# Performance work log

Measured on AMD Instinct MI355X. Metric: run time of the kernel, lower is better.

## Reference

```python
import jax, jax.numpy as jnp
import numpy as np

B, C, H, W = 16, 256, 56, 56
PH, PW = 7, 7            # partition (window) size
HEADS, DH = 8, 32        # n_heads = C // head_dim
P = PH * PW              # tokens per window = 49
GH, GW = H // PH, W // PW
G = GH * GW              # number of windows = 64
MLP = 4                  # mlp_ratio
EPS = 1e-5
SCALE = C ** (-0.5)      # note: torch code scales by feat_dim, not head_dim


def _rel_index(h, w):
    coords = np.stack(np.meshgrid(np.arange(h), np.arange(w), indexing='ij'))  # [2,h,w]
    cf = coords.reshape(2, -1)
    rel = cf[:, :, None] - cf[:, None, :]              # [2,P,P]
    rel = rel.transpose(1, 2, 0)
    rel[:, :, 0] += h - 1
    rel[:, :, 1] += w - 1
    rel[:, :, 0] *= 2 * w - 1
    return rel.sum(-1).astype(np.int32)                # [P,P]


def setup_inputs() -> dict:
    key = jax.random.key(0)
    ks = jax.random.split(key, 8)
    std = 0.02
    return {
        'x': jax.random.normal(ks[0], (B, C, H, W), jnp.float32),
        'ln1_g': jnp.ones((C,), jnp.float32),
        'ln1_b': jnp.zeros((C,), jnp.float32),
        'wqkv': jax.random.normal(ks[1], (C, 3 * C), jnp.float32) * std,
        'bqkv': jnp.zeros((3 * C,), jnp.float32),
        'wmerge': jax.random.normal(ks[2], (C, C), jnp.float32) * std,
        'bmerge': jnp.zeros((C,), jnp.float32),
        'bias_table': jax.random.normal(ks[3], ((2 * PH - 1) * (2 * PW - 1), HEADS), jnp.float32) * std,
        'ln2_g': jnp.ones((C,), jnp.float32),
        'ln2_b': jnp.zeros((C,), jnp.float32),
        'w1': jax.random.normal(ks[4], (C, MLP * C), jnp.float32) * std,
        'b1': jnp.zeros((MLP * C,), jnp.float32),
        'w2': jax.random.normal(ks[5], (MLP * C, C), jnp.float32) * std,
        'b2': jnp.zeros((C,), jnp.float32),
        'rel_idx': jnp.asarray(_rel_index(PH, PW)),
    }


def _layernorm(x, g, b):
    mu = jnp.mean(x, axis=-1, keepdims=True)
    var = jnp.var(x, axis=-1, keepdims=True)
    return (x - mu) * jax.lax.rsqrt(var + EPS) * g + b


def reference(x, ln1_g, ln1_b, wqkv, bqkv, wmerge, bmerge, bias_table,
              ln2_g, ln2_b, w1, b1, w2, b2, rel_idx):
    # --- window partition: [B,C,H,W] -> [B,G,P,C]
    xw = x.reshape(B, C, GH, PH, GW, PW).transpose(0, 2, 4, 3, 5, 1).reshape(B, G, P, C)

    # --- relative-position attention block
    y = _layernorm(xw, ln1_g, ln1_b)
    qkv = y @ wqkv + bqkv                               # [B,G,P,3C]
    q, k, v = jnp.split(qkv, 3, axis=-1)
    q = q.reshape(B, G, P, HEADS, DH)
    k = k.reshape(B, G, P, HEADS, DH) * SCALE
    v = v.reshape(B, G, P, HEADS, DH)
    scores = jnp.einsum('bgihd,bgjhd->bghij', q, k)     # [B,G,H,P,P]
    bias = bias_table[rel_idx].transpose(2, 0, 1)       # [H,P,P]
    attn = jax.nn.softmax(scores + bias[None, None], axis=-1)
    out = jnp.einsum('bghij,bgjhd->bgihd', attn, v).reshape(B, G, P, C)
    out = out @ wmerge + bmerge
    xw = xw + out

    # --- MLP block
    z = _layernorm(xw, ln2_g, ln2_b)
    z = jax.nn.gelu(z @ w1 + b1, approximate=False) @ w2 + b2
    xw = xw + z

    # --- window departition: [B,G,P,C] -> [B,C,H,W]
    xo = xw.reshape(B, GH, GW, PH, PW, C).transpose(0, 5, 1, 3, 2, 4).reshape(B, C, H, W)
    return xo
```

## Files before the change

kernel.cpp:

```cpp
#include <hip/hip_runtime.h>
#include <hip/hip_bf16.h>

#define B_      16
#define C_      256
#define H_      56
#define W_      56
#define HW_     3136
#define G_      64
#define P_      49
#define NTOK    50176
#define HEADS_  8
#define DH_     32
#define SCALE_  0.0625f
#define EPS_    1e-5f

typedef short bf16x8 __attribute__((ext_vector_type(8)));
typedef short bf16x4_t __attribute__((ext_vector_type(4)));
typedef float f32x4  __attribute__((ext_vector_type(4)));
using bf16 = __hip_bfloat16;

__device__ __forceinline__ void gload16(const void* g, void* l) {
  __builtin_amdgcn_global_load_lds((const __attribute__((address_space(1))) void*)g,
                                   (__attribute__((address_space(3))) void*)l, 16, 0, 0);
}
__device__ __forceinline__ float b2f(short s) {
  union { float f; unsigned u; } v; v.u = ((unsigned)(unsigned short)s) << 16; return v.f;
}
__device__ __forceinline__ short f2b(float f) {
  union { float f; unsigned u; } v; v.f = f;
  unsigned r = (v.u + 0x7FFFu + ((v.u >> 16) & 1u)) >> 16;
  return (short)r;
}

__global__ __launch_bounds__(256)
void prep_kernel(const float* __restrict__ wqkv, const float* __restrict__ wmerge,
                 const float* __restrict__ w1, const float* __restrict__ w2,
                 const float* __restrict__ btab, const int* __restrict__ relidx,
                 bf16* __restrict__ wqkvT, bf16* __restrict__ wmergeT,
                 bf16* __restrict__ w1T, bf16* __restrict__ w2T,
                 short* __restrict__ bt)
{
  int idx = blockIdx.x * 256 + threadIdx.x;
  if (idx < 196608) { int n = idx >> 8, k = idx & 255;
    wqkvT[idx] = __float2bfloat16(wqkv[k * 768 + n]); return; }
  idx -= 196608;
  if (idx < 65536) { int n = idx >> 8, k = idx & 255;
    wmergeT[idx] = __float2bfloat16(wmerge[k * 256 + n]); return; }
  idx -= 65536;
  if (idx < 262144) { int n = idx >> 8, k = idx & 255;
    w1T[idx] = __float2bfloat16(w1[k * 1024 + n]); return; }
  idx -= 262144;
  if (idx < 262144) { int n = idx >> 10, k = idx & 1023;
    w2T[idx] = __float2bfloat16(w2[k * 256 + n]); return; }
  idx -= 262144;
  if (idx < 32768) {
    int h = idx >> 12, rest = idx & 4095;
    int key = rest >> 6, col = rest & 63;
    int q = col >> 2, qni = col & 3;
    int query = qni * 16 + q;
    float v = 0.f;
    if (key < P_ && query < P_) v = btab[relidx[query * P_ + key] * HEADS_ + h];
    bt[idx] = f2b(v);
  }
}

__global__ __launch_bounds__(256)
void ingest_kernel(const float* __restrict__ x, const float* __restrict__ gam,
                   const float* __restrict__ bet, short* __restrict__ xtok,
                   short* __restrict__ y)
{
  __shared__ short Lt[56 * 260];
  const int h = blockIdx.x % 56, b = blockIdx.x / 56;
  const int tid = threadIdx.x;

  const float* xb = x + (size_t)b * 256 * HW_ + h * 56;
#pragma unroll
  for (int i = 0; i < 14; i++) {
    int idx = i * 256 + tid;
    int c = idx / 14, w4 = idx - c * 14;
    float4 v = *(const float4*)(xb + (size_t)c * HW_ + w4 * 4);
    Lt[(w4 * 4 + 0) * 260 + c] = f2b(v.x);
    Lt[(w4 * 4 + 1) * 260 + c] = f2b(v.y);
    Lt[(w4 * 4 + 2) * 260 + c] = f2b(v.z);
    Lt[(w4 * 4 + 3) * 260 + c] = f2b(v.w);
  }
  __syncthreads();

  const int lane = tid & 63, wv = tid >> 6;
  float4 gv = *(const float4*)(gam + lane * 4);
  float4 bv = *(const float4*)(bet + lane * 4);
  const int hdiv = h / 7, hmod = h - hdiv * 7;

  for (int t = 0; t < 14; t++) {
    int w = wv * 14 + t;
    bf16x4_t raw = *(const bf16x4_t*)&Lt[w * 260 + lane * 4];
    float f0 = b2f(raw[0]), f1 = b2f(raw[1]), f2 = b2f(raw[2]), f3 = b2f(raw[3]);
    float sum = f0 + f1 + f2 + f3;
    float sq  = f0*f0 + f1*f1 + f2*f2 + f3*f3;
#pragma unroll
    for (int off = 32; off > 0; off >>= 1) {
      sum += __shfl_xor(sum, off, 64);
      sq  += __shfl_xor(sq,  off, 64);
    }
    float mu = sum * (1.0f / 256.0f);
    float var = sq * (1.0f / 256.0f) - mu * mu;
    float rs = rsqrtf(var + EPS_);
    int wdiv = w / 7, wmod = w - wdiv * 7;
    int tok = b * HW_ + (hdiv * 8 + wdiv) * P_ + hmod * 7 + wmod;
    *(bf16x4_t*)(xtok + (size_t)tok * 256 + lane * 4) = raw;
    bf16x4_t o;
    o[0] = f2b((f0 - mu) * rs * gv.x + bv.x);
    o[1] = f2b((f1 - mu) * rs * gv.y + bv.y);
    o[2] = f2b((f2 - mu) * rs * gv.z + bv.z);
    o[3] = f2b((f3 - mu) * rs * gv.w + bv.w);
    *(bf16x4_t*)(y + (size_t)tok * 256 + lane * 4) = o;
  }
}

__global__ __launch_bounds__(256)
void egress_kernel(const short* __restrict__ outtok, float* __restrict__ out)
{
  const int h = blockIdx.x % 56, b = blockIdx.x / 56;
  const int w = threadIdx.x & 63, cblk = threadIdx.x >> 6;
  const bool act = w < 56;
  const int wcl = act ? w : 55;
  const int tok = b * HW_ + ((h / 7) * 8 + wcl / 7) * P_ + (h % 7) * 7 + (wcl % 7);
  const short* src = outtok + (size_t)tok * 256 + cblk * 64;
  float* dst = out + ((size_t)b * 256 + cblk * 64) * HW_ + h * 56 + w;
#pragma unroll
  for (int j0 = 0; j0 < 64; j0 += 8) {
    bf16x8 r = *(const bf16x8*)(src + j0);
#pragma unroll
    for (int jj = 0; jj < 8; jj++)
      if (act) dst[(size_t)(j0 + jj) * HW_] = b2f(r[jj]);
  }
}

__global__ __launch_bounds__(64)
void attn_kernel(const short* __restrict__ qkv, const short* __restrict__ bt,
                 short* __restrict__ out)
{
  __shared__ short Pbuf[64 * 72];
  const int bid = blockIdx.x;
  const int h = bid & 7;
  const int t0 = (bid >> 3) * P_;
  const int lane = threadIdx.x;
  const int g = lane >> 4, q = lane & 15;

  const short* qb = qkv + (size_t)t0 * 768 + h * 32;

  bf16x8 vf[2][2];
#pragma unroll
  for (int kkt = 0; kkt < 2; kkt++)
#pragma unroll
    for (int n2 = 0; n2 < 2; n2++)
#pragma unroll
      for (int jj = 0; jj < 8; jj++) {
        int key = kkt * 32 + 8 * g + jj; key = key > 48 ? 48 : key;
        vf[kkt][n2][jj] = qb[(size_t)key * 768 + 512 + n2 * 16 + q];
      }

  bf16x8 kf[4], qf[4];
#pragma unroll
  for (int mi = 0; mi < 4; mi++) {
    int r_ = mi * 16 + q; r_ = r_ > 48 ? 48 : r_;
    kf[mi] = *(const bf16x8*)(qb + (size_t)r_ * 768 + 256 + 8 * g);
  }
#pragma unroll
  for (int ni = 0; ni < 4; ni++) {
    int r_ = ni * 16 + q; r_ = r_ > 48 ? 48 : r_;
    qf[ni] = *(const bf16x8*)(qb + (size_t)r_ * 768 + 8 * g);
  }

  f32x4 sacc[4][4] = {};
#pragma unroll
  for (int mi = 0; mi < 4; mi++)
#pragma unroll
    for (int ni = 0; ni < 4; ni++)
      sacc[mi][ni] = __builtin_amdgcn_mfma_f32_16x16x32_bf16(kf[mi], qf[ni], sacc[mi][ni], 0, 0, 0);

  float mx[4] = {-1e30f, -1e30f, -1e30f, -1e30f};
  const short* btb = bt + (size_t)(h * 64) * 64 + q * 4;
#pragma unroll
  for (int mi = 0; mi < 4; mi++)
#pragma unroll
    for (int r = 0; r < 4; r++) {
      int key = mi * 16 + 4 * g + r;
      bf16x4_t bv = *(const bf16x4_t*)(btb + key * 64);
      bool valid = key < P_;
#pragma unroll
      for (int ni = 0; ni < 4; ni++) {
        float s = valid ? fmaf(sacc[mi][ni][r], SCALE_, b2f(bv[ni])) : -1e30f;
        sacc[mi][ni][r] = s;
        mx[ni] = fmaxf(mx[ni], s);
      }
    }
#pragma unroll
  for (int ni = 0; ni < 4; ni++) {
    mx[ni] = fmaxf(mx[ni], __shfl_xor(mx[ni], 16, 64));
    mx[ni] = fmaxf(mx[ni], __shfl_xor(mx[ni], 32, 64));
  }
  float sm[4] = {0.f, 0.f, 0.f, 0.f};
#pragma unroll
  for (int mi = 0; mi < 4; mi++)
#pragma unroll
    for (int ni = 0; ni < 4; ni++)
#pragma unroll
      for (int r = 0; r < 4; r++) {
        float p = __expf(sacc[mi][ni][r] - mx[ni]);
        sacc[mi][ni][r] = p;
        sm[ni] += p;
      }
#pragma unroll
  for (int ni = 0; ni < 4; ni++) {
    sm[ni] += __shfl_xor(sm[ni], 16, 64);
    sm[ni] += __shfl_xor(sm[ni], 32, 64);
    sm[ni] = 1.0f / sm[ni];
  }
#pragma unroll
  for (int ni = 0; ni < 4; ni++)
#pragma unroll
    for (int mi = 0; mi < 4; mi++) {
      bf16x4_t pv;
#pragma unroll
      for (int r = 0; r < 4; r++) pv[r] = f2b(sacc[mi][ni][r] * sm[ni]);
      *(bf16x4_t*)&Pbuf[(ni * 16 + q) * 72 + mi * 16 + 4 * g] = pv;
    }
  __syncthreads();

  f32x4 oacc[4][2] = {};
#pragma unroll
  for (int kkt = 0; kkt < 2; kkt++) {
    bf16x8 paf[4];
#pragma unroll
    for (int qi = 0; qi < 4; qi++)
      paf[qi] = *(const bf16x8*)&Pbuf[(qi * 16 + q) * 72 + kkt * 32 + 8 * g];
#pragma unroll
    for (int qi = 0; qi < 4; qi++)
#pragma unroll
      for (int n2 = 0; n2 < 2; n2++)
        oacc[qi][n2] = __builtin_amdgcn_mfma_f32_16x16x32_bf16(paf[qi], vf[kkt][n2], oacc[qi][n2], 0, 0, 0);
  }

  short* ob = out + (size_t)t0 * 256 + h * 32;
#pragma unroll
  for (int qi = 0; qi < 4; qi++)
#pragma unroll
    for (int r = 0; r < 4; r++) {
      int query = qi * 16 + 4 * g + r;
      if (query < P_) {
#pragma unroll
        for (int n2 = 0; n2 < 2; n2++)
          ob[(size_t)query * 256 + n2 * 16 + q] = f2b(oacc[qi][n2][r]);
      }
    }
}

template<int EPI, int WR, int WN>
__global__ __launch_bounds__(WR * WN * 64)
void gemm_kernel(const bf16* __restrict__ A, const bf16* __restrict__ Wt,
                 const float* __restrict__ bias, int N, int K,
                 bf16* __restrict__ outb, short* __restrict__ res_io,
                 short* __restrict__ z_out,
                 const float* __restrict__ gam, const float* __restrict__ bet)
{
  constexpr int THREADS = WR * WN * 64;
  constexpr int BM = WR * 64, BN = WN * 64;
  constexpr int RPP = THREADS / 4;
  constexpr int APASS = BM / RPP > 0 ? BM / RPP : 1;
  constexpr int BPASS = BN / RPP > 0 ? BN / RPP : 1;
  __shared__ __align__(16) bf16 As[2][BM * 32];
  __shared__ __align__(16) bf16 Bs[2][BN * 32];
  __shared__ float red1[(EPI == 3) ? 64 : 1][(EPI == 3) ? WN : 1];
  __shared__ float red2[(EPI == 3) ? 64 : 1][(EPI == 3) ? WN : 1];

  const int tid = threadIdx.x;
  const int lane = tid & 63;
  const int wave = tid >> 6;
  const int wr = wave / WN, wc = wave % WN;

  int bx = blockIdx.x, by = blockIdx.y;
  {
    const int gx = gridDim.x, gy = gridDim.y;
    if (gx > 1) {
      int hwid = blockIdx.x + gx * blockIdx.y;
      int band = gx * 8;
      int fullb = gy >> 3;
      int full = fullb * band;
      if (hwid < full) {
        int g8 = hwid / band, w = hwid % band;
        by = g8 * 8 + (w & 7); bx = w >> 3;
      } else {
        int rem = gy & 7;
        int w = hwid - full;
        by = fullb * 8 + w % rem; bx = w / rem;
      }
    }
  }
  const int bm = by * BM, bn = bx * BN;

  f32x4 acc[4][4] = {};

  const int trow = tid >> 2;
  const int tcol = ((tid & 3) ^ ((tid >> 3) & 3)) * 8;
  const bf16* aA[APASS];
  const bf16* aB[BPASS];
#pragma unroll
  for (int p = 0; p < APASS; p++)
    aA[p] = A + (size_t)(bm + p * RPP + trow) * K + tcol;
#pragma unroll
  for (int p = 0; p < BPASS; p++)
    aB[p] = Wt + (size_t)(bn + p * RPP + trow) * K + tcol;
  const int dOff = tid * 8;

  const int kc_sw = ((lane >> 4) ^ ((lane >> 1) & 3)) * 8;
  const int l15 = lane & 15, g = lane >> 4;
  const int rA = wr * 64 + l15;
  const int rB = wc * 64 + l15;

  const int nt = K >> 5;

#pragma unroll
  for (int p = 0; p < APASS; p++) gload16(aA[p], &As[0][p * RPP * 32 + dOff]);
#pragma unroll
  for (int p = 0; p < BPASS; p++) gload16(aB[p], &Bs[0][p * RPP * 32 + dOff]);
  __syncthreads();

  for (int t = 0; t < nt; ++t) {
    const int cur = t & 1;
    if (t + 1 < nt) {
      const int k1 = (t + 1) << 5;
      const int nxt = cur ^ 1;
#pragma unroll
      for (int p = 0; p < APASS; p++) gload16(aA[p] + k1, &As[nxt][p * RPP * 32 + dOff]);
#pragma unroll
      for (int p = 0; p < BPASS; p++) gload16(aB[p] + k1, &Bs[nxt][p * RPP * 32 + dOff]);
    }
    bf16x8 af[4], bfr[4];
#pragma unroll
    for (int i = 0; i < 4; i++) {
      af[i]  = *(const bf16x8*)(&As[cur][(rA + i * 16) * 32 + kc_sw]);
      bfr[i] = *(const bf16x8*)(&Bs[cur][(rB + i * 16) * 32 + kc_sw]);
    }
#pragma unroll
    for (int mi = 0; mi < 4; mi++)
#pragma unroll
      for (int ni = 0; ni < 4; ni++)
        acc[mi][ni] = __builtin_amdgcn_mfma_f32_16x16x32_bf16(af[mi], bfr[ni], acc[mi][ni], 0, 0, 0);
    __syncthreads();
  }

  if constexpr (EPI == 3) {
    const int ocol0 = wc * 64;
    float bv[4], gv[4], btv[4];
#pragma unroll
    for (int ni = 0; ni < 4; ni++) {
      bv[ni]  = bias[ocol0 + ni * 16 + l15];
      gv[ni]  = gam[ocol0 + ni * 16 + l15];
      btv[ni] = bet[ocol0 + ni * 16 + l15];
    }
#pragma unroll
    for (int mi = 0; mi < 4; mi++)
#pragma unroll
      for (int r = 0; r < 4; r++) {
        const int rowl = mi * 16 + g * 4 + r;
        float s1 = 0.f, s2 = 0.f;
#pragma unroll
        for (int ni = 0; ni < 4; ni++) {
          const int col = ocol0 + ni * 16 + l15;
          float v = acc[mi][ni][r] + bv[ni]
                  + b2f(res_io[(size_t)(bm + rowl) * 256 + col]);
          acc[mi][ni][r] = v;
          s1 += v; s2 += v * v;
        }
#pragma unroll
        for (int off = 1; off < 16; off <<= 1) {
          s1 += __shfl_xor(s1, off, 64);
          s2 += __shfl_xor(s2, off, 64);
        }
        if (l15 == 0) { red1[rowl][wc] = s1; red2[rowl][wc] = s2; }
      }
    __syncthreads();
#pragma unroll
    for (int mi = 0; mi < 4; mi++)
#pragma unroll
      for (int r = 0; r < 4; r++) {
        const int rowl = mi * 16 + g * 4 + r;
        float m1 = 0.f, m2 = 0.f;
#pragma unroll
        for (int j = 0; j < WN; j++) { m1 += red1[rowl][j]; m2 += red2[rowl][j]; }
        float mu = m1 * (1.0f / 256.0f);
        float var = m2 * (1.0f / 256.0f) - mu * mu;
        float rs = rsqrtf(var + EPS_);
#pragma unroll
        for (int ni = 0; ni < 4; ni++) {
          const int col = ocol0 + ni * 16 + l15;
          float v = acc[mi][ni][r];
          res_io[(size_t)(bm + rowl) * 256 + col] = f2b(v);
          z_out [(size_t)(bm + rowl) * 256 + col] = f2b((v - mu) * rs * gv[ni] + btv[ni]);
        }
      }
    return;
  }

#pragma unroll
  for (int mi = 0; mi < 4; mi++) {
#pragma unroll
    for (int ni = 0; ni < 4; ni++) {
#pragma unroll
      for (int r = 0; r < 4; r++) {
        const int row = bm + wr * 64 + mi * 16 + g * 4 + r;
        const int col = bn + wc * 64 + ni * 16 + l15;
        float v = acc[mi][ni][r] + bias[col];
        if (EPI == 0) {
          outb[(size_t)row * N + col] = __float2bfloat16(v);
        } else if (EPI == 1) {
          float u = 0.7978845608f * v * (1.0f + 0.044715f * v * v);
          float e = __expf(2.0f * u);
          float th = 1.0f - 2.0f / (e + 1.0f);
          outb[(size_t)row * N + col] = __float2bfloat16(0.5f * v * (1.0f + th));
        } else {
          size_t o = (size_t)row * 256 + col;
          res_io[o] = f2b(v + b2f(res_io[o]));
        }
      }
    }
  }
}

extern "C" void kernel_launch(void* const* d_in, const int* in_sizes, int n_in,
                              void* d_out, int out_size, void* d_ws, size_t ws_size,
                              hipStream_t stream)
{
  const float* x      = (const float*)d_in[0];
  const float* ln1_g  = (const float*)d_in[1];
  const float* ln1_b  = (const float*)d_in[2];
  const float* wqkv   = (const float*)d_in[3];
  const float* bqkv   = (const float*)d_in[4];
  const float* wmerge = (const float*)d_in[5];
  const float* bmerge = (const float*)d_in[6];
  const float* btab   = (const float*)d_in[7];
  const float* ln2_g  = (const float*)d_in[8];
  const float* ln2_b  = (const float*)d_in[9];
  const float* w1     = (const float*)d_in[10];
  const float* b1     = (const float*)d_in[11];
  const float* w2     = (const float*)d_in[12];
  const float* b2     = (const float*)d_in[13];
  const int*   relidx = (const int*)d_in[14];
  float* out = (float*)d_out;

  char* ws = (char*)d_ws;
  bf16*  wqkvT   = (bf16*)(ws);
  bf16*  wmergeT = (bf16*)(ws + 393216);
  bf16*  w1T     = (bf16*)(ws + 524288);
  bf16*  w2T     = (bf16*)(ws + 1048576);
  short* battn   = (short*)(ws + 1572864);
  short* R1      = (short*)(ws + 1638400);
  short* R2      = (short*)(ws + 27328512);
  short* qkvc    = (short*)(ws + 53018624);
  short* attnc   = (short*)(ws + 91553792);
  short* hbuf    = (short*)(ws + 53018624);

  prep_kernel<<<3200, 256, 0, stream>>>(wqkv, wmerge, w1, w2, btab, relidx,
                                        wqkvT, wmergeT, w1T, w2T, battn);

  ingest_kernel<<<896, 256, 0, stream>>>(x, ln1_g, ln1_b, R1, R2);

  for (int c = 0; c < 2; ++c) {
    size_t r0 = (size_t)c * 25088;
    gemm_kernel<0, 2, 4><<<dim3(3, 196), 512, 0, stream>>>(
        (const bf16*)(R2 + r0 * 256), wqkvT, bqkv, 768, 256, (bf16*)qkvc,
        nullptr, nullptr, nullptr, nullptr);
    attn_kernel<<<4096, 64, 0, stream>>>(qkvc, battn, attnc);
    gemm_kernel<3, 1, 4><<<dim3(1, 392), 256, 0, stream>>>(
        (const bf16*)attnc, wmergeT, bmerge, 256, 256, nullptr,
        R1 + r0 * 256, R2 + r0 * 256, ln2_g, ln2_b);
  }

  for (int c = 0; c < 2; ++c) {
    size_t r0 = (size_t)c * 25088;
    gemm_kernel<1, 2, 4><<<dim3(4, 196), 512, 0, stream>>>(
        (const bf16*)(R2 + r0 * 256), w1T, b1, 1024, 256, (bf16*)hbuf,
        nullptr, nullptr, nullptr, nullptr);
    gemm_kernel<2, 2, 2><<<dim3(2, 196), 256, 0, stream>>>(
        (const bf16*)hbuf, w2T, b2, 256, 1024, nullptr,
        R1 + r0 * 256, nullptr, nullptr, nullptr);
  }

  egress_kernel<<<896, 256, 0, stream>>>(R1, out);
}
```

Measured before the change: 322.9 us.

## Load GEMM MFMA fragments directly from global memory instead of LDS staging

Result: slower. 481.7 us (+49.2%).

```diff
diff --git a/kernel.cpp b/kernel.cpp
--- a/kernel.cpp
+++ b/kernel.cpp
@@ -19,17 +19,12 @@
 typedef float f32x4  __attribute__((ext_vector_type(4)));
 using bf16 = __hip_bfloat16;
 
-__device__ __forceinline__ void gload16(const void* g, void* l) {
-  __builtin_amdgcn_global_load_lds((const __attribute__((address_space(1))) void*)g,
-                                   (__attribute__((address_space(3))) void*)l, 16, 0, 0);
-}
 __device__ __forceinline__ float b2f(short s) {
   union { float f; unsigned u; } v; v.u = ((unsigned)(unsigned short)s) << 16; return v.f;
 }
 __device__ __forceinline__ short f2b(float f) {
-  union { float f; unsigned u; } v; v.f = f;
-  unsigned r = (v.u + 0x7FFFu + ((v.u >> 16) & 1u)) >> 16;
-  return (short)r;
+  __hip_bfloat16 h = __float2bfloat16(f);
+  return *reinterpret_cast<short*>(&h);
 }
 
 __global__ __launch_bounds__(256)
@@ -256,21 +251,15 @@
     }
 }
 
-template<int EPI, int WR, int WN>
+template<int EPI, int WR, int WN, int K>
 __global__ __launch_bounds__(WR * WN * 64)
 void gemm_kernel(const bf16* __restrict__ A, const bf16* __restrict__ Wt,
-                 const float* __restrict__ bias, int N, int K,
-                 bf16* __restrict__ outb, short* __restrict__ res_io,
-                 short* __restrict__ z_out,
+                 const float* __restrict__ bias, int N,
+                 bf16* __restrict__ outb, bf16* __restrict__ res_io,
+                 bf16* __restrict__ z_out,
                  const float* __restrict__ gam, const float* __restrict__ bet)
 {
-  constexpr int THREADS = WR * WN * 64;
   constexpr int BM = WR * 64, BN = WN * 64;
-  constexpr int RPP = THREADS / 4;
-  constexpr int APASS = BM / RPP > 0 ? BM / RPP : 1;
-  constexpr int BPASS = BN / RPP > 0 ? BN / RPP : 1;
-  __shared__ __align__(16) bf16 As[2][BM * 32];
-  __shared__ __align__(16) bf16 Bs[2][BN * 32];
   __shared__ float red1[(EPI == 3) ? 64 : 1][(EPI == 3) ? WN : 1];
   __shared__ float red2[(EPI == 3) ? 64 : 1][(EPI == 3) ? WN : 1];
 
@@ -278,6 +267,7 @@
   const int lane = tid & 63;
   const int wave = tid >> 6;
   const int wr = wave / WN, wc = wave % WN;
+  const int l15 = lane & 15, g = lane >> 4;
 
   int bx = blockIdx.x, by = blockIdx.y;
   {
@@ -299,55 +289,32 @@
   }
   const int bm = by * BM, bn = bx * BN;
 
+  const bf16* Ap[4];
+  const bf16* Bp[4];
+#pragma unroll
+  for (int mi = 0; mi < 4; mi++)
+    Ap[mi] = A + (size_t)(bm + wr * 64 + mi * 16 + l15) * K + g * 8;
+#pragma unroll
+  for (int ni = 0; ni < 4; ni++)
+    Bp[ni] = Wt + (size_t)(bn + wc * 64 + ni * 16 + l15) * K + g * 8;
+
   f32x4 acc[4][4] = {};
 
-  const int trow = tid >> 2;
-  const int tcol = ((tid & 3) ^ ((tid >> 3) & 3)) * 8;
-  const bf16* aA[APASS];
-  const bf16* aB[BPASS];
-#pragma unroll
-  for (int p = 0; p < APASS; p++)
-    aA[p] = A + (size_t)(bm + p * RPP + trow) * K + tcol;
-#pragma unroll
-  for (int p = 0; p < BPASS; p++)
-    aB[p] = Wt + (size_t)(bn + p * RPP + trow) * K + tcol;
-  const int dOff = tid * 8;
-
-  const int kc_sw = ((lane >> 4) ^ ((lane >> 1) & 3)) * 8;
-  const int l15 = lane & 15, g = lane >> 4;
-  const int rA = wr * 64 + l15;
-  const int rB = wc * 64 + l15;
-
-  const int nt = K >> 5;
-
-#pragma unroll
-  for (int p = 0; p < APASS; p++) gload16(aA[p], &As[0][p * RPP * 32 + dOff]);
-#pragma unroll
-  for (int p = 0; p < BPASS; p++) gload16(aB[p], &Bs[0][p * RPP * 32 + dOff]);
-  __syncthreads();
-
-  for (int t = 0; t < nt; ++t) {
-    const int cur = t & 1;
-    if (t + 1 < nt) {
-      const int k1 = (t + 1) << 5;
-      const int nxt = cur ^ 1;
-#pragma unroll
-      for (int p = 0; p < APASS; p++) gload16(aA[p] + k1, &As[nxt][p * RPP * 32 + dOff]);
-#pragma unroll
-      for (int p = 0; p < BPASS; p++) gload16(aB[p] + k1, &Bs[nxt][p * RPP * 32 + dOff]);
-    }
-    bf16x8 af[4], bfr[4];
-#pragma unroll
-    for (int i = 0; i < 4; i++) {
-      af[i]  = *(const bf16x8*)(&As[cur][(rA + i * 16) * 32 + kc_sw]);
-      bfr[i] = *(const bf16x8*)(&Bs[cur][(rB + i * 16) * 32 + kc_sw]);
-    }
-#pragma unroll
-    for (int mi = 0; mi < 4; mi++)
-#pragma unroll
-      for (int ni = 0; ni < 4; ni++)
-        acc[mi][ni] = __builtin_amdgcn_mfma_f32_16x16x32_bf16(af[mi], bfr[ni], acc[mi][ni], 0, 0, 0);
-    __syncthreads();
+  for (int k0 = 0; k0 < K; k0 += 256) {
+#pragma unroll
+    for (int t = 0; t < 8; ++t) {
+      const int k = k0 + t * 32;
+      bf16x8 af[4], bfr[4];
+#pragma unroll
+      for (int mi = 0; mi < 4; mi++) af[mi] = *(const bf16x8*)(Ap[mi] + k);
+#pragma unroll
+      for (int ni = 0; ni < 4; ni++) bfr[ni] = *(const bf16x8*)(Bp[ni] + k);
+#pragma unroll
+      for (int mi = 0; mi < 4; mi++)
+#pragma unroll
+        for (int ni = 0; ni < 4; ni++)
+          acc[mi][ni] = __builtin_amdgcn_mfma_f32_16x16x32_bf16(af[mi], bfr[ni], acc[mi][ni], 0, 0, 0);
+    }
   }
 
   if constexpr (EPI == 3) {
@@ -369,7 +336,7 @@
         for (int ni = 0; ni < 4; ni++) {
           const int col = ocol0 + ni * 16 + l15;
           float v = acc[mi][ni][r] + bv[ni]
-                  + b2f(res_io[(size_t)(bm + rowl) * 256 + col]);
+                  + __bfloat162float(res_io[(size_t)(bm + rowl) * 256 + col]);
           acc[mi][ni][r] = v;
           s1 += v; s2 += v * v;
         }
@@ -396,8 +363,9 @@
         for (int ni = 0; ni < 4; ni++) {
           const int col = ocol0 + ni * 16 + l15;
           float v = acc[mi][ni][r];
-          res_io[(size_t)(bm + rowl) * 256 + col] = f2b(v);
-          z_out [(size_t)(bm + rowl) * 256 + col] = f2b((v - mu) * rs * gv[ni] + btv[ni]);
+          res_io[(size_t)(bm + rowl) * 256 + col] = __float2bfloat16(v);
+          z_out [(size_t)(bm + rowl) * 256 + col] =
+              __float2bfloat16((v - mu) * rs * gv[ni] + btv[ni]);
         }
       }
     return;
@@ -407,11 +375,12 @@
   for (int mi = 0; mi < 4; mi++) {
 #pragma unroll
     for (int ni = 0; ni < 4; ni++) {
+      const int col = bn + wc * 64 + ni * 16 + l15;
+      const float bv = bias[col];
 #pragma unroll
       for (int r = 0; r < 4; r++) {
         const int row = bm + wr * 64 + mi * 16 + g * 4 + r;
-        const int col = bn + wc * 64 + ni * 16 + l15;
-        float v = acc[mi][ni][r] + bias[col];
+        float v = acc[mi][ni][r] + bv;
         if (EPI == 0) {
           outb[(size_t)row * N + col] = __float2bfloat16(v);
         } else if (EPI == 1) {
@@ -421,7 +390,7 @@
           outb[(size_t)row * N + col] = __float2bfloat16(0.5f * v * (1.0f + th));
         } else {
           size_t o = (size_t)row * 256 + col;
-          res_io[o] = f2b(v + b2f(res_io[o]));
+          res_io[o] = __float2bfloat16(v + __bfloat162float(res_io[o]));
         }
       }
     }
@@ -468,23 +437,23 @@
 
   for (int c = 0; c < 2; ++c) {
     size_t r0 = (size_t)c * 25088;
-    gemm_kernel<0, 2, 4><<<dim3(3, 196), 512, 0, stream>>>(
-        (const bf16*)(R2 + r0 * 256), wqkvT, bqkv, 768, 256, (bf16*)qkvc,
+    gemm_kernel<0, 2, 2, 256><<<dim3(6, 196), 256, 0, stream>>>(
+        (const bf16*)(R2 + r0 * 256), wqkvT, bqkv, 768, (bf16*)qkvc,
         nullptr, nullptr, nullptr, nullptr);
     attn_kernel<<<4096, 64, 0, stream>>>(qkvc, battn, attnc);
-    gemm_kernel<3, 1, 4><<<dim3(1, 392), 256, 0, stream>>>(
-        (const bf16*)attnc, wmergeT, bmerge, 256, 256, nullptr,
-        R1 + r0 * 256, R2 + r0 * 256, ln2_g, ln2_b);
+    gemm_kernel<3, 1, 4, 256><<<dim3(1, 392), 256, 0, stream>>>(
+        (const bf16*)attnc, wmergeT, bmerge, 256, nullptr,
+        (bf16*)(R1 + r0 * 256), (bf16*)(R2 + r0 * 256), ln2_g, ln2_b);
   }
 
   for (int c = 0; c < 2; ++c) {
     size_t r0 = (size_t)c * 25088;
-    gemm_kernel<1, 2, 4><<<dim3(4, 196), 512, 0, stream>>>(
-        (const bf16*)(R2 + r0 * 256), w1T, b1, 1024, 256, (bf16*)hbuf,
+    gemm_kernel<1, 2, 2, 256><<<dim3(8, 196), 256, 0, stream>>>(
+        (const bf16*)(R2 + r0 * 256), w1T, b1, 1024, (bf16*)hbuf,
         nullptr, nullptr, nullptr, nullptr);
-    gemm_kernel<2, 2, 2><<<dim3(2, 196), 256, 0, stream>>>(
-        (const bf16*)hbuf, w2T, b2, 256, 1024, nullptr,
-        R1 + r0 * 256, nullptr, nullptr, nullptr);
+    gemm_kernel<2, 2, 2, 1024><<<dim3(2, 196), 256, 0, stream>>>(
+        (const bf16*)hbuf, w2T, b2, 256, nullptr,
+        (bf16*)(R1 + r0 * 256), nullptr, nullptr, nullptr);
   }
 
   egress_kernel<<<896, 256, 0, stream>>>(R1, out);
```
